# Performance work log

Measured on AMD Instinct MI355X. Metric: run time of the kernel, lower is better.

## Reference

```python
import jax, jax.numpy as jnp
import numpy as np

D_MODEL = 1024
NHEAD = 16
HEAD_DIM = D_MODEL // NHEAD


def setup_inputs() -> dict:
    key = jax.random.key(0)
    k_x, k_wqkv, k_bqkv, k_wo, k_bo = jax.random.split(key, 5)
    scale_in = 1.0 / np.sqrt(D_MODEL)
    x = jax.random.normal(k_x, (2, 2048, D_MODEL), dtype=jnp.float32)
    # qkv_proj: Linear(d_model, 3*d_model); stored as [in, out] for x @ W
    W_qkv = jax.random.uniform(k_wqkv, (D_MODEL, 3 * D_MODEL), dtype=jnp.float32,
                               minval=-scale_in, maxval=scale_in)
    b_qkv = jax.random.uniform(k_bqkv, (3 * D_MODEL,), dtype=jnp.float32,
                               minval=-scale_in, maxval=scale_in)
    W_out = jax.random.uniform(k_wo, (D_MODEL, D_MODEL), dtype=jnp.float32,
                               minval=-scale_in, maxval=scale_in)
    b_out = jax.random.uniform(k_bo, (D_MODEL,), dtype=jnp.float32,
                               minval=-scale_in, maxval=scale_in)
    return {"x": x, "W_qkv": W_qkv, "b_qkv": b_qkv, "W_out": W_out, "b_out": b_out}


def reference(x, W_qkv, b_qkv, W_out, b_out):
    B, S, _ = x.shape
    qkv = x @ W_qkv + b_qkv                                   # [B,S,3*d_model]
    # Faithful to torch module: reshape to [B,S,H,3*hd], move heads, chunk LAST dim
    qkv = qkv.reshape(B, S, NHEAD, 3 * HEAD_DIM)
    qkv = qkv.transpose(0, 2, 1, 3)                            # [B,H,S,3*hd]
    q, k, v = jnp.split(qkv, 3, axis=-1)                       # each [B,H,S,hd]
    scale = 1.0 / np.sqrt(HEAD_DIM).astype(np.float32)
    attn = jnp.einsum('bhqd,bhkd->bhqk', q, k) * scale         # [B,H,S,S]
    attn = jax.nn.softmax(attn, axis=-1)
    out = jnp.einsum('bhqk,bhkd->bhqd', attn, v)               # [B,H,S,hd]
    out = out.transpose(0, 2, 1, 3).reshape(B, S, D_MODEL)     # [B,S,d_model]
    return out @ W_out + b_out
```

## Files before the change

### kernel.cpp

```cpp
#include <hip/hip_runtime.h>
#include <cmath>

typedef unsigned short u16;
typedef unsigned int u32;
typedef __bf16 bf16x8 __attribute__((ext_vector_type(8)));
typedef float f32x4 __attribute__((ext_vector_type(4)));

#define D_MODEL 1024
#define NHEAD 16
#define HD 64
#define SEQ 2048
#define BATCH 2
#define M_TOK 4096
#define N_QKV 3072

#define LOG2E 1.4426950408889634f
#define SOFTMAX_SHIFT 11.541560327111707f

__device__ __forceinline__ u16 f2bf(float f) {
    u32 u = __float_as_uint(f);
    u32 r = (u + 0x7fffu + ((u >> 16) & 1u)) >> 16;
    return (u16)r;
}

__device__ __forceinline__ float bf2f(u16 v) {
    return __uint_as_float(((u32)v) << 16);
}

__device__ __forceinline__ u32 pack_bf(float a, float b) {
#if __has_builtin(__builtin_amdgcn_cvt_pk_bf16_f32)
    typedef __bf16 bf16x2_t __attribute__((ext_vector_type(2)));
    union { bf16x2_t v; u32 u; } c;
    c.v = __builtin_amdgcn_cvt_pk_bf16_f32(a, b);
    return c.u;
#else
    u32 ua = __float_as_uint(a) + 0x8000u;
    u32 ub = __float_as_uint(b) + 0x8000u;
    return __builtin_amdgcn_perm(ub, ua, 0x07060302u);
#endif
}

__device__ __forceinline__ bf16x8 ld_bf8(const u16* p) {
    return *(const bf16x8*)p;
}

__device__ __forceinline__ bf16x8 as_bf8(int4 v) {
    union { int4 i; bf16x8 b; } u; u.i = v; return u.b;
}

__device__ __forceinline__ f32x4 mfma16(bf16x8 a, bf16x8 b, f32x4 c) {
    return __builtin_amdgcn_mfma_f32_16x16x32_bf16(a, b, c, 0, 0, 0);
}

__device__ __forceinline__ void gload_lds16(const u16* g, u16* l) {
    __builtin_amdgcn_global_load_lds(
        (const __attribute__((address_space(1))) void*)g,
        (__attribute__((address_space(3))) void*)l, 16, 0, 0);
}

__device__ __forceinline__ int Gv(int x) {
    int q = x / 192, rm = x - q * 192;
    int e = rm - 128;
    return q * 64 + (e > 0 ? e : 0);
}

__global__ void cast_x_kernel(const float* __restrict__ in, u16* __restrict__ out, int n4) {
    int i = blockIdx.x * blockDim.x + threadIdx.x;
    int stride = gridDim.x * blockDim.x;
    for (; i < n4; i += stride) {
        float4 v = ((const float4*)in)[i];
        ushort4 o;
        o.x = f2bf(v.x); o.y = f2bf(v.y); o.z = f2bf(v.z); o.w = f2bf(v.w);
        ((ushort4*)out)[i] = o;
    }
}

template <int ROWS, int COLS>
__global__ void transpose_cast_kernel(const float* __restrict__ in, u16* __restrict__ out) {
    __shared__ float tile[32][33];
    int c0 = blockIdx.x * 32;
    int r0 = blockIdx.y * 32;
    int tx = threadIdx.x;
    int ty = threadIdx.y;
#pragma unroll
    for (int i = 0; i < 32; i += 8)
        tile[ty + i][tx] = in[(size_t)(r0 + ty + i) * COLS + c0 + tx];
    __syncthreads();
#pragma unroll
    for (int i = 0; i < 32; i += 8)
        out[(size_t)(c0 + ty + i) * ROWS + r0 + tx] = f2bf(tile[tx][ty + i]);
}

__global__ __launch_bounds__(256) void gemm_qkv_kernel(
    const u16* __restrict__ A, const u16* __restrict__ Bt, const float* __restrict__ bias,
    u16* __restrict__ Qb, u16* __restrict__ Kb, u16* __restrict__ Vp)
{
    __shared__ u16 lA[128 * 32];
    __shared__ u16 lB[128 * 32];
    __shared__ u16 vtile[64 * 132];
    int w = threadIdx.x >> 6, l = threadIdx.x & 63;
    int col = l & 15, quad = l >> 4;
    int wm = w >> 1, wn = w & 1;
    int m0 = blockIdx.x * 128;
    int n0 = blockIdx.y * 128;
    int lrow = l >> 2;
    int lcol = (l & 3) * 8;

    f32x4 acc[4][4] = {};
    for (int k0 = 0; k0 < 1024; k0 += 32) {
        __syncthreads();
#pragma unroll
        for (int i = 0; i < 2; i++) {
            int slab = w * 32 + i * 16;
            gload_lds16(A  + (size_t)(m0 + slab + lrow) * 1024 + k0 + lcol, lA + slab * 32);
            gload_lds16(Bt + (size_t)(n0 + slab + lrow) * 1024 + k0 + lcol, lB + slab * 32);
        }
        __syncthreads();
        bf16x8 af[4], bfr[4];
#pragma unroll
        for (int i = 0; i < 4; i++)
            af[i] = ld_bf8(lA + (wm * 64 + i * 16 + col) * 32 + quad * 8);
#pragma unroll
        for (int j = 0; j < 4; j++)
            bfr[j] = ld_bf8(lB + (wn * 64 + j * 16 + col) * 32 + quad * 8);
#pragma unroll
        for (int i = 0; i < 4; i++)
#pragma unroll
            for (int j = 0; j < 4; j++)
                acc[i][j] = mfma16(af[i], bfr[j], acc[i][j]);
    }

    int s0 = m0 & 2047;
    int bblk = m0 >> 11;
#pragma unroll
    for (int i = 0; i < 4; i++) {
#pragma unroll
        for (int j = 0; j < 4; j++) {
            int cc = n0 + wn * 64 + j * 16 + col;
            int h = cc / 192;
            int within = cc - h * 192;
            int ww = within >> 6;
            int d = within & 63;
            int vloc = Gv(cc) - Gv(n0);
            float bv = bias[cc];
#pragma unroll
            for (int r = 0; r < 4; r++) {
                int sloc = wm * 64 + i * 16 + quad * 4 + r;
                int s = s0 + sloc;
                int bh = bblk * NHEAD + h;
                float val = acc[i][j][r] + bv;
                if (ww == 0)      Qb[(size_t)(bh * SEQ + s) * HD + d] = f2bf(val * 0.125f);
                else if (ww == 1) Kb[(size_t)(bh * SEQ + s) * HD + d] = f2bf(val);
                else {
                    int sp = (sloc & ~31) | ((sloc & 12) << 1) | (((sloc >> 4) & 1) << 2) | (sloc & 3);
                    vtile[vloc * 132 + sp] = f2bf(val);
                }
            }
        }
    }
    __syncthreads();
    int vcols = Gv(n0 + 128) - Gv(n0);
    int gbase = Gv(n0);
    for (int c = threadIdx.x; c < vcols * 16; c += 256) {
        int vloc = c >> 4, gi = c & 15;
        int av = gbase + vloc;
        int h = av >> 6, d = av & 63;
        int bh = bblk * NHEAD + h;
        int4 vv = *(const int4*)(vtile + vloc * 132 + gi * 8);
        *(int4*)(Vp + ((size_t)(bh * HD + d)) * SEQ + s0 + gi * 8) = vv;
    }
}

__global__ __launch_bounds__(256, 4) void attn_kernel(
    const u16* __restrict__ Qb, const u16* __restrict__ Kb,
    const u16* __restrict__ Vp, u16* __restrict__ O0,
    u16* __restrict__ O1, float* __restrict__ Lp)
{
    __shared__ u16 kbuf[2][64 * 64];
    __shared__ u16 vbuf[2][64 * 64];
    int wave = threadIdx.x >> 6, lane = threadIdx.x & 63;
    int col = lane & 15, quad = lane >> 4;
    int g = blockIdx.x;
    int xcd = g & 7, slot = g >> 3;
    int bh = xcd * 4 + (slot >> 5);
    int rem = slot & 31;
    int split = rem >> 4;
    int qt = rem & 15;
    int q0 = qt * 128 + wave * 32;
    int kstart = split * 16;

    int srow = lane >> 3;
    int sgrp = (lane & 7) ^ srow;
    const u16* Kt0 = Kb + (size_t)bh * SEQ * HD;
    const u16* Vt0 = Vp + (size_t)bh * HD * SEQ;
    long soffK = (long)srow * HD + sgrp * 8;
    long soffV = (long)srow * SEQ + sgrp * 8;
    int r0 = wave * 16;

    int rbase = col * 64;
    int sw0 = ((quad)     ^ (col & 7)) * 8;
    int sw1 = ((quad + 4) ^ (col & 7)) * 8;

    union { u32 w[4]; int4 i; } onesu;
    onesu.w[0] = onesu.w[1] = onesu.w[2] = onesu.w[3] = 0x3F803F80u;
    bf16x8 ones = as_bf8(onesu.i);

    bf16x8 aq[2][2];
#pragma unroll
    for (int m = 0; m < 2; m++) {
        const u16* qbase = Qb + ((size_t)bh * SEQ + q0 + m * 16 + col) * HD + quad * 8;
        aq[m][0] = ld_bf8(qbase);
        aq[m][1] = ld_bf8(qbase + 32);
    }

    f32x4 o[2][4] = {};
    f32x4 ol[2] = {};

    {
        int kbase = kstart * 64;
        gload_lds16(Kt0 + (size_t)(kbase + r0) * HD + soffK,      kbuf[0] + r0 * 64);
        gload_lds16(Kt0 + (size_t)(kbase + r0 + 8) * HD + soffK,  kbuf[0] + (r0 + 8) * 64);
        gload_lds16(Vt0 + (size_t)r0 * SEQ + kbase + soffV,       vbuf[0] + r0 * 64);
        gload_lds16(Vt0 + (size_t)(r0 + 8) * SEQ + kbase + soffV, vbuf[0] + (r0 + 8) * 64);
    }

    for (int kt = 0; kt < 16; ++kt) {
        int cur = kt & 1;
        __syncthreads();
        if (kt + 1 < 16) {
            int kbase = (kstart + kt + 1) * 64;
            int nb = cur ^ 1;
            gload_lds16(Kt0 + (size_t)(kbase + r0) * HD + soffK,      kbuf[nb] + r0 * 64);
            gload_lds16(Kt0 + (size_t)(kbase + r0 + 8) * HD + soffK,  kbuf[nb] + (r0 + 8) * 64);
            gload_lds16(Vt0 + (size_t)r0 * SEQ + kbase + soffV,       vbuf[nb] + r0 * 64);
            gload_lds16(Vt0 + (size_t)(r0 + 8) * SEQ + kbase + soffV, vbuf[nb] + (r0 + 8) * 64);
        }
        const u16* kb = kbuf[cur];
        const u16* vb = vbuf[cur];
        bf16x8 kf[4][2];
#pragma unroll
        for (int t = 0; t < 4; t++) {
            kf[t][0] = ld_bf8(kb + t * 1024 + rbase + sw0);
            kf[t][1] = ld_bf8(kb + t * 1024 + rbase + sw1);
        }
        int4 vraw[4][2];
#pragma unroll
        for (int t = 0; t < 4; t++) {
            vraw[t][0] = *(const int4*)(vb + t * 1024 + rbase + sw0);
            vraw[t][1] = *(const int4*)(vb + t * 1024 + rbase + sw1);
        }
        int4 pfrag[2][2];
#pragma unroll
        for (int m = 0; m < 2; m++) {
#pragma unroll
            for (int t = 0; t < 4; t++) {
                f32x4 sa = {};
                sa = mfma16(kf[t][0], aq[m][0], sa);
                sa = mfma16(kf[t][1], aq[m][1], sa);
                f32x4 p;
#pragma unroll
                for (int r = 0; r < 4; r++)
                    p[r] = __builtin_exp2f(__builtin_fmaf(sa[r], LOG2E, -SOFTMAX_SHIFT));
                u32 lo = pack_bf(p[0], p[1]);
                u32 hi = pack_bf(p[2], p[3]);
                if ((t & 1) == 0) { pfrag[m][t >> 1].x = (int)lo; pfrag[m][t >> 1].y = (int)hi; }
                else              { pfrag[m][t >> 1].z = (int)lo; pfrag[m][t >> 1].w = (int)hi; }
            }
        }
#pragma unroll
        for (int m = 0; m < 2; m++) {
#pragma unroll
            for (int t = 0; t < 4; t++)
#pragma unroll
                for (int h = 0; h < 2; h++)
                    o[m][t] = mfma16(as_bf8(pfrag[m][h]), as_bf8(vraw[t][h]), o[m][t]);
            ol[m] = mfma16(as_bf8(pfrag[m][0]), ones, ol[m]);
            ol[m] = mfma16(as_bf8(pfrag[m][1]), ones, ol[m]);
        }
    }

    u16* Op = split ? O1 : O0;
#pragma unroll
    for (int m = 0; m < 2; m++) {
#pragma unroll
        for (int r = 0; r < 4; r++) {
            int srow2 = q0 + m * 16 + quad * 4 + r;
            if (col == 0)
                Lp[(size_t)split * 32 * SEQ + (size_t)bh * SEQ + srow2] = ol[m][r];
#pragma unroll
            for (int t = 0; t < 4; t++)
                Op[((size_t)bh * SEQ + srow2) * HD + t * 16 + col] = f2bf(o[m][t][r]);
        }
    }
}

__global__ __launch_bounds__(256) void combine_kernel(
    const u16* __restrict__ O0, const u16* __restrict__ O1,
    const float* __restrict__ Lp, u16* __restrict__ At)
{
    int i = blockIdx.x * 256 + threadIdx.x;
    int dg = i & 15;
    int q = (i >> 4) & 2047;
    int bh = i >> 15;
    size_t ob = ((size_t)bh * SEQ + q) * HD + dg * 4;
    ushort4 a = *(const ushort4*)(O0 + ob);
    ushort4 b = *(const ushort4*)(O1 + ob);
    float l = Lp[(size_t)bh * SEQ + q] + Lp[(size_t)32 * SEQ + (size_t)bh * SEQ + q];
    float inv = 1.f / l;
    int bb = bh >> 4, h = bh & 15;
    ushort4 o;
    o.x = f2bf((bf2f(a.x) + bf2f(b.x)) * inv);
    o.y = f2bf((bf2f(a.y) + bf2f(b.y)) * inv);
    o.z = f2bf((bf2f(a.z) + bf2f(b.z)) * inv);
    o.w = f2bf((bf2f(a.w) + bf2f(b.w)) * inv);
    *(ushort4*)(At + ((size_t)(bb * SEQ + q)) * D_MODEL + h * 64 + dg * 4) = o;
}

__global__ __launch_bounds__(256) void gemm_out_kernel(
    const u16* __restrict__ A, const u16* __restrict__ Bt, const float* __restrict__ bias,
    float* __restrict__ out)
{
    __shared__ u16 lA[128 * 32];
    __shared__ u16 lB[128 * 32];
    int w = threadIdx.x >> 6, l = threadIdx.x & 63;
    int col = l & 15, quad = l >> 4;
    int wm = w >> 1, wn = w & 1;
    int m0 = blockIdx.x * 128;
    int n0 = blockIdx.y * 128;
    int lrow = l >> 2;
    int lcol = (l & 3) * 8;

    f32x4 acc[4][4] = {};
    for (int k0 = 0; k0 < 1024; k0 += 32) {
        __syncthreads();
#pragma unroll
        for (int i = 0; i < 2; i++) {
            int slab = w * 32 + i * 16;
            gload_lds16(A  + (size_t)(m0 + slab + lrow) * 1024 + k0 + lcol, lA + slab * 32);
            gload_lds16(Bt + (size_t)(n0 + slab + lrow) * 1024 + k0 + lcol, lB + slab * 32);
        }
        __syncthreads();
        bf16x8 af[4], bfr[4];
#pragma unroll
        for (int i = 0; i < 4; i++)
            af[i] = ld_bf8(lA + (wm * 64 + i * 16 + col) * 32 + quad * 8);
#pragma unroll
        for (int j = 0; j < 4; j++)
            bfr[j] = ld_bf8(lB + (wn * 64 + j * 16 + col) * 32 + quad * 8);
#pragma unroll
        for (int i = 0; i < 4; i++)
#pragma unroll
            for (int j = 0; j < 4; j++)
                acc[i][j] = mfma16(af[i], bfr[j], acc[i][j]);
    }

#pragma unroll
    for (int i = 0; i < 4; i++) {
#pragma unroll
        for (int j = 0; j < 4; j++) {
            int cc = n0 + wn * 64 + j * 16 + col;
            float bv = bias[cc];
#pragma unroll
            for (int r = 0; r < 4; r++) {
                int row = m0 + wm * 64 + i * 16 + quad * 4 + r;
                out[(size_t)row * D_MODEL + cc] = acc[i][j][r] + bv;
            }
        }
    }
}

extern "C" void kernel_launch(void* const* d_in, const int* in_sizes, int n_in,
                              void* d_out, int out_size, void* d_ws, size_t ws_size,
                              hipStream_t stream) {
    const float* x     = (const float*)d_in[0];
    const float* W_qkv = (const float*)d_in[1];
    const float* b_qkv = (const float*)d_in[2];
    const float* W_out = (const float*)d_in[3];
    const float* b_out = (const float*)d_in[4];
    float* out = (float*)d_out;

    char* ws = (char*)d_ws;
    u16* Xb    = (u16*)(ws);
    u16* Wqkvt = (u16*)(ws + (8ull << 20));
    u16* Qb    = (u16*)(ws + (16ull << 20));
    u16* Kb    = (u16*)(ws + (24ull << 20));
    u16* Vp    = (u16*)(ws + (32ull << 20));
    u16* O0    = (u16*)(ws);
    u16* O1    = (u16*)(ws + (8ull << 20));
    float* Lp  = (float*)(ws + (40ull << 20));
    u16* At    = (u16*)(ws + (16ull << 20));
    u16* Woutt = (u16*)(ws);

    cast_x_kernel<<<1024, 256, 0, stream>>>(x, Xb, M_TOK * D_MODEL / 4);
    transpose_cast_kernel<1024, 3072><<<dim3(96, 32), dim3(32, 8), 0, stream>>>(W_qkv, Wqkvt);
    gemm_qkv_kernel<<<dim3(32, 24), 256, 0, stream>>>(Xb, Wqkvt, b_qkv, Qb, Kb, Vp);
    attn_kernel<<<dim3(1024), 256, 0, stream>>>(Qb, Kb, Vp, O0, O1, Lp);
    combine_kernel<<<dim3(BATCH * NHEAD * SEQ * (HD / 4) / 256), 256, 0, stream>>>(O0, O1, Lp, At);
    transpose_cast_kernel<1024, 1024><<<dim3(32, 32), dim3(32, 8), 0, stream>>>(W_out, Woutt);
    gemm_out_kernel<<<dim3(32, 8), 256, 0, stream>>>(At, Woutt, b_out, out);
}
```

Before: 208.5 us.

## Fuse input casts into one prep kernel and double-buffer GEMM LDS tiles

Merges the x cast and both weight transpose-casts into a single launch, and moves the W_out copy to its own workspace region so it can be written up front. Both GEMMs now double-buffer their LDS A/B tiles: the next K-slab is issued before the MFMAs on the current slab, and one barrier per iteration is dropped. This aims to cut launch overhead and hide global-to-LDS latency, at the cost of doubled shared memory per block. It relies on global_load_lds completing before the next barrier without an explicit wait, which may be a correctness risk.

```diff
diff --git a/kernel.cpp b/kernel.cpp
--- a/kernel.cpp
+++ b/kernel.cpp
@@ -64,24 +64,39 @@
     return q * 64 + (e > 0 ? e : 0);
 }
 
-__global__ void cast_x_kernel(const float* __restrict__ in, u16* __restrict__ out, int n4) {
-    int i = blockIdx.x * blockDim.x + threadIdx.x;
-    int stride = gridDim.x * blockDim.x;
-    for (; i < n4; i += stride) {
-        float4 v = ((const float4*)in)[i];
-        ushort4 o;
-        o.x = f2bf(v.x); o.y = f2bf(v.y); o.z = f2bf(v.z); o.w = f2bf(v.w);
-        ((ushort4*)out)[i] = o;
-    }
-}
-
-template <int ROWS, int COLS>
-__global__ void transpose_cast_kernel(const float* __restrict__ in, u16* __restrict__ out) {
+__global__ __launch_bounds__(256) void prep_kernel(
+    const float* __restrict__ x, u16* __restrict__ Xb,
+    const float* __restrict__ W_qkv, u16* __restrict__ Wqkvt,
+    const float* __restrict__ W_out, u16* __restrict__ Woutt)
+{
+    int blk = blockIdx.x;
+    if (blk < 1024) {
+        int n4 = M_TOK * D_MODEL / 4;
+        int i = blk * 256 + threadIdx.x;
+        int stride = 1024 * 256;
+        for (; i < n4; i += stride) {
+            float4 v = ((const float4*)x)[i];
+            ushort4 o;
+            o.x = f2bf(v.x); o.y = f2bf(v.y); o.z = f2bf(v.z); o.w = f2bf(v.w);
+            ((ushort4*)Xb)[i] = o;
+        }
+        return;
+    }
     __shared__ float tile[32][33];
-    int c0 = blockIdx.x * 32;
-    int r0 = blockIdx.y * 32;
-    int tx = threadIdx.x;
-    int ty = threadIdx.y;
+    const float* in;
+    u16* out;
+    int ROWS, COLS, bx, by;
+    if (blk < 4096) {
+        int b = blk - 1024;
+        bx = b % 96; by = b / 96;
+        in = W_qkv; out = Wqkvt; ROWS = 1024; COLS = 3072;
+    } else {
+        int b = blk - 4096;
+        bx = b & 31; by = b >> 5;
+        in = W_out; out = Woutt; ROWS = 1024; COLS = 1024;
+    }
+    int c0 = bx * 32, r0 = by * 32;
+    int tx = threadIdx.x & 31, ty = threadIdx.x >> 5;
 #pragma unroll
     for (int i = 0; i < 32; i += 8)
         tile[ty + i][tx] = in[(size_t)(r0 + ty + i) * COLS + c0 + tx];
@@ -95,8 +110,8 @@
     const u16* __restrict__ A, const u16* __restrict__ Bt, const float* __restrict__ bias,
     u16* __restrict__ Qb, u16* __restrict__ Kb, u16* __restrict__ Vp)
 {
-    __shared__ u16 lA[128 * 32];
-    __shared__ u16 lB[128 * 32];
+    __shared__ u16 lA[2][128 * 32];
+    __shared__ u16 lB[2][128 * 32];
     __shared__ u16 vtile[64 * 132];
     int w = threadIdx.x >> 6, l = threadIdx.x & 63;
     int col = l & 15, quad = l >> 4;
@@ -106,23 +121,34 @@
     int lrow = l >> 2;
     int lcol = (l & 3) * 8;
 
+#pragma unroll
+    for (int i = 0; i < 2; i++) {
+        int slab = w * 32 + i * 16;
+        gload_lds16(A  + (size_t)(m0 + slab + lrow) * 1024 + lcol, lA[0] + slab * 32);
+        gload_lds16(Bt + (size_t)(n0 + slab + lrow) * 1024 + lcol, lB[0] + slab * 32);
+    }
+
     f32x4 acc[4][4] = {};
-    for (int k0 = 0; k0 < 1024; k0 += 32) {
+    for (int it = 0; it < 32; ++it) {
+        int cur = it & 1;
         __syncthreads();
-#pragma unroll
-        for (int i = 0; i < 2; i++) {
-            int slab = w * 32 + i * 16;
-            gload_lds16(A  + (size_t)(m0 + slab + lrow) * 1024 + k0 + lcol, lA + slab * 32);
-            gload_lds16(Bt + (size_t)(n0 + slab + lrow) * 1024 + k0 + lcol, lB + slab * 32);
-        }
-        __syncthreads();
+        if (it + 1 < 32) {
+            int k0 = (it + 1) * 32;
+            int nb = cur ^ 1;
+#pragma unroll
+            for (int i = 0; i < 2; i++) {
+                int slab = w * 32 + i * 16;
+                gload_lds16(A  + (size_t)(m0 + slab + lrow) * 1024 + k0 + lcol, lA[nb] + slab * 32);
+                gload_lds16(Bt + (size_t)(n0 + slab + lrow) * 1024 + k0 + lcol, lB[nb] + slab * 32);
+            }
+        }
         bf16x8 af[4], bfr[4];
 #pragma unroll
         for (int i = 0; i < 4; i++)
-            af[i] = ld_bf8(lA + (wm * 64 + i * 16 + col) * 32 + quad * 8);
+            af[i] = ld_bf8(lA[cur] + (wm * 64 + i * 16 + col) * 32 + quad * 8);
 #pragma unroll
         for (int j = 0; j < 4; j++)
-            bfr[j] = ld_bf8(lB + (wn * 64 + j * 16 + col) * 32 + quad * 8);
+            bfr[j] = ld_bf8(lB[cur] + (wn * 64 + j * 16 + col) * 32 + quad * 8);
 #pragma unroll
         for (int i = 0; i < 4; i++)
 #pragma unroll
@@ -320,8 +346,8 @@
     const u16* __restrict__ A, const u16* __restrict__ Bt, const float* __restrict__ bias,
     float* __restrict__ out)
 {
-    __shared__ u16 lA[128 * 32];
-    __shared__ u16 lB[128 * 32];
+    __shared__ u16 lA[2][128 * 32];
+    __shared__ u16 lB[2][128 * 32];
     int w = threadIdx.x >> 6, l = threadIdx.x & 63;
     int col = l & 15, quad = l >> 4;
     int wm = w >> 1, wn = w & 1;
@@ -330,23 +356,34 @@
     int lrow = l >> 2;
     int lcol = (l & 3) * 8;
 
+#pragma unroll
+    for (int i = 0; i < 2; i++) {
+        int slab = w * 32 + i * 16;
+        gload_lds16(A  + (size_t)(m0 + slab + lrow) * 1024 + lcol, lA[0] + slab * 32);
+        gload_lds16(Bt + (size_t)(n0 + slab + lrow) * 1024 + lcol, lB[0] + slab * 32);
+    }
+
     f32x4 acc[4][4] = {};
-    for (int k0 = 0; k0 < 1024; k0 += 32) {
+    for (int it = 0; it < 32; ++it) {
+        int cur = it & 1;
         __syncthreads();
-#pragma unroll
-        for (int i = 0; i < 2; i++) {
-            int slab = w * 32 + i * 16;
-            gload_lds16(A  + (size_t)(m0 + slab + lrow) * 1024 + k0 + lcol, lA + slab * 32);
-            gload_lds16(Bt + (size_t)(n0 + slab + lrow) * 1024 + k0 + lcol, lB + slab * 32);
-        }
-        __syncthreads();
+        if (it + 1 < 32) {
+            int k0 = (it + 1) * 32;
+            int nb = cur ^ 1;
+#pragma unroll
+            for (int i = 0; i < 2; i++) {
+                int slab = w * 32 + i * 16;
+                gload_lds16(A  + (size_t)(m0 + slab + lrow) * 1024 + k0 + lcol, lA[nb] + slab * 32);
+                gload_lds16(Bt + (size_t)(n0 + slab + lrow) * 1024 + k0 + lcol, lB[nb] + slab * 32);
+            }
+        }
         bf16x8 af[4], bfr[4];
 #pragma unroll
         for (int i = 0; i < 4; i++)
-            af[i] = ld_bf8(lA + (wm * 64 + i * 16 + col) * 32 + quad * 8);
+            af[i] = ld_bf8(lA[cur] + (wm * 64 + i * 16 + col) * 32 + quad * 8);
 #pragma unroll
         for (int j = 0; j < 4; j++)
-            bfr[j] = ld_bf8(lB + (wn * 64 + j * 16 + col) * 32 + quad * 8);
+            bfr[j] = ld_bf8(lB[cur] + (wn * 64 + j * 16 + col) * 32 + quad * 8);
 #pragma unroll
         for (int i = 0; i < 4; i++)
 #pragma unroll
@@ -388,14 +425,12 @@
     u16* O0    = (u16*)(ws);
     u16* O1    = (u16*)(ws + (8ull << 20));
     float* Lp  = (float*)(ws + (40ull << 20));
+    u16* Woutt = (u16*)(ws + (41ull << 20));
     u16* At    = (u16*)(ws + (16ull << 20));
-    u16* Woutt = (u16*)(ws);
-
-    cast_x_kernel<<<1024, 256, 0, stream>>>(x, Xb, M_TOK * D_MODEL / 4);
-    transpose_cast_kernel<1024, 3072><<<dim3(96, 32), dim3(32, 8), 0, stream>>>(W_qkv, Wqkvt);
+
+    prep_kernel<<<dim3(5120), 256, 0, stream>>>(x, Xb, W_qkv, Wqkvt, W_out, Woutt);
     gemm_qkv_kernel<<<dim3(32, 24), 256, 0, stream>>>(Xb, Wqkvt, b_qkv, Qb, Kb, Vp);
     attn_kernel<<<dim3(1024), 256, 0, stream>>>(Qb, Kb, Vp, O0, O1, Lp);
     combine_kernel<<<dim3(BATCH * NHEAD * SEQ * (HD / 4) / 256), 256, 0, stream>>>(O0, O1, Lp, At);
-    transpose_cast_kernel<1024, 1024><<<dim3(32, 32), dim3(32, 8), 0, stream>>>(W_out, Woutt);
     gemm_out_kernel<<<dim3(32, 8), 256, 0, stream>>>(At, Woutt, b_out, out);
 }
```

Result: slower. 212.8 us (+2.0%).
